# Kernel tuning notes

Measured on AMD Instinct MI355X. Metric: run time of the kernel, lower is better.

## Reference

```python
import jax, jax.numpy as jnp
import numpy as np

TQ, B, H = 1024, 16, 1024   # decoder steps, batch, hidden
S = 4096                     # encoder length


def setup_inputs() -> dict:
    key = jax.random.key(0)
    k1, k2 = jax.random.split(key)
    hiddenState = jax.random.normal(k1, (TQ, B, H), dtype=jnp.float32)
    encoderOut = jax.random.normal(k2, (S, B, H), dtype=jnp.float32)
    return {"hiddenState": hiddenState, "encoderOut": encoderOut}


def reference(hiddenState, encoderOut):
    # encoderOut: [S,B,H] -> [B,S,H]; hiddenState: [Tq,B,H] -> [B,Tq,H]
    # scores[b,s,t] = sum_h enc[b,s,h] * hid[b,t,h]  (bmm of [B,S,H] x [B,H,Tq])
    scores = jnp.einsum('sbh,tbh->bst', encoderOut, hiddenState)  # [B,S,Tq]
    attW = jax.nn.softmax(jnp.tanh(scores), axis=1)  # softmax over encoder axis S
    return attW
```

## Files before the change

kernel.cpp:

```cpp
#include <hip/hip_runtime.h>
#include <hip/hip_bf16.h>

#define TQn 1024
#define Bn  16
#define Hn  1024
#define Sn  4096

#define BM 128
#define BN 128
#define BK 64
#define NKS (Hn / BK)

typedef _Float16 f16x8 __attribute__((ext_vector_type(8)));
typedef float    f32x4 __attribute__((ext_vector_type(4)));

__device__ __forceinline__ void cvt_split(const f32x4& v0, const f32x4& v1,
                                          f16x8& hi, f16x8& lo) {
#pragma unroll
  for (int e = 0; e < 4; ++e) {
    _Float16 h = (_Float16)v0[e];
    hi[e] = h;
    lo[e] = (_Float16)(v0[e] - (float)h);
  }
#pragma unroll
  for (int e = 0; e < 4; ++e) {
    _Float16 h = (_Float16)v1[e];
    hi[4 + e] = h;
    lo[4 + e] = (_Float16)(v1[e] - (float)h);
  }
}

__global__ __launch_bounds__(256, 2)
void att_gemm(const float* __restrict__ hid,
              const float* __restrict__ enc,
              float* __restrict__ out,
              float* __restrict__ sums)
{
  __shared__ f16x8 sAhi[BM * BK / 8];
  __shared__ f16x8 sAlo[BM * BK / 8];
  __shared__ f16x8 sBhi[BN * BK / 8];
  __shared__ f16x8 sBlo[BN * BK / 8];

  const int tid  = threadIdx.x;
  const int lane = tid & 63;
  const int wv   = tid >> 6;
  const int wm   = (wv >> 1) << 6;
  const int wn   = (wv & 1) << 6;

  const int b  = blockIdx.z;
  const int s0 = blockIdx.y * BM;
  const int t0 = blockIdx.x * BN;

  const int unit = tid & 7;
  const int row0 = tid >> 3;

  const float* encB = enc + (size_t)b * Hn;
  const float* hidB = hid + (size_t)b * Hn;
  const size_t ldg = (size_t)Bn * Hn;

  f32x4 acc[4][4];
#pragma unroll
  for (int m = 0; m < 4; ++m)
#pragma unroll
    for (int n = 0; n < 4; ++n)
      acc[m][n] = (f32x4){0.f, 0.f, 0.f, 0.f};

  f32x4 ra[4][2], rb[4][2];

#pragma unroll
  for (int i = 0; i < 4; ++i) {
    const float* pa = encB + (size_t)(s0 + row0 + 32 * i) * ldg + unit * 8;
    ra[i][0] = *(const f32x4*)pa;
    ra[i][1] = *(const f32x4*)(pa + 4);
    const float* pb = hidB + (size_t)(t0 + row0 + 32 * i) * ldg + unit * 8;
    rb[i][0] = *(const f32x4*)pb;
    rb[i][1] = *(const f32x4*)(pb + 4);
  }
#pragma unroll
  for (int i = 0; i < 4; ++i) {
    const int row = row0 + 32 * i;
    const int u   = unit ^ (row & 7);
    f16x8 hi, lo;
    cvt_split(ra[i][0], ra[i][1], hi, lo);
    sAhi[row * 8 + u] = hi;
    sAlo[row * 8 + u] = lo;
    cvt_split(rb[i][0], rb[i][1], hi, lo);
    sBhi[row * 8 + u] = hi;
    sBlo[row * 8 + u] = lo;
  }
  __syncthreads();

#pragma unroll 1
  for (int ks = 0; ks < NKS; ++ks) {
    if (ks + 1 < NKS) {
      const int ko = (ks + 1) * BK;
#pragma unroll
      for (int i = 0; i < 4; ++i) {
        const float* pa = encB + (size_t)(s0 + row0 + 32 * i) * ldg + ko + unit * 8;
        ra[i][0] = *(const f32x4*)pa;
        ra[i][1] = *(const f32x4*)(pa + 4);
        const float* pb = hidB + (size_t)(t0 + row0 + 32 * i) * ldg + ko + unit * 8;
        rb[i][0] = *(const f32x4*)pb;
        rb[i][1] = *(const f32x4*)(pb + 4);
      }
    }

#pragma unroll
    for (int sl = 0; sl < 2; ++sl) {
      const int ko = sl * 4 + (lane >> 4);
      f16x8 ah[4], al[4], bh[4], bl[4];
#pragma unroll
      for (int m = 0; m < 4; ++m) {
        const int r = wm + m * 16 + (lane & 15);
        const int u = ko ^ (r & 7);
        ah[m] = sAhi[r * 8 + u];
        al[m] = sAlo[r * 8 + u];
      }
#pragma unroll
      for (int n = 0; n < 4; ++n) {
        const int r = wn + n * 16 + (lane & 15);
        const int u = ko ^ (r & 7);
        bh[n] = sBhi[r * 8 + u];
        bl[n] = sBlo[r * 8 + u];
      }
#pragma unroll
      for (int m = 0; m < 4; ++m)
#pragma unroll
        for (int n = 0; n < 4; ++n) {
          acc[m][n] = __builtin_amdgcn_mfma_f32_16x16x32_f16(ah[m], bh[n], acc[m][n], 0, 0, 0);
          acc[m][n] = __builtin_amdgcn_mfma_f32_16x16x32_f16(ah[m], bl[n], acc[m][n], 0, 0, 0);
          acc[m][n] = __builtin_amdgcn_mfma_f32_16x16x32_f16(al[m], bh[n], acc[m][n], 0, 0, 0);
        }
    }
    __syncthreads();

    if (ks + 1 < NKS) {
#pragma unroll
      for (int i = 0; i < 4; ++i) {
        const int row = row0 + 32 * i;
        const int u   = unit ^ (row & 7);
        f16x8 hi, lo;
        cvt_split(ra[i][0], ra[i][1], hi, lo);
        sAhi[row * 8 + u] = hi;
        sAlo[row * 8 + u] = lo;
        cvt_split(rb[i][0], rb[i][1], hi, lo);
        sBhi[row * 8 + u] = hi;
        sBlo[row * 8 + u] = lo;
      }
    }
    __syncthreads();
  }

#pragma unroll
  for (int n = 0; n < 4; ++n) {
    const int t = t0 + wn + n * 16 + (lane & 15);
    float csum = 0.f;
#pragma unroll
    for (int m = 0; m < 4; ++m) {
      const int sb = s0 + wm + m * 16 + ((lane >> 4) << 2);
#pragma unroll
      for (int j = 0; j < 4; ++j) {
        const float x  = acc[m][n][j];
        const float w  = __expf(tanhf(x));
        out[((size_t)b * Sn + (sb + j)) * TQn + t] = w;
        csum += w;
      }
    }
    csum += __shfl_xor(csum, 16, 64);
    csum += __shfl_xor(csum, 32, 64);
    if ((lane >> 4) == 0)
      atomicAdd(&sums[b * TQn + t], csum);
  }
}

__global__ void zero_kernel(float* __restrict__ p, int n) {
  int i = blockIdx.x * 256 + threadIdx.x;
  if (i < n) p[i] = 0.f;
}

__global__ void inv_kernel(float* __restrict__ sums, int n) {
  int i = blockIdx.x * 256 + threadIdx.x;
  if (i < n) sums[i] = 1.0f / sums[i];
}

__global__ __launch_bounds__(256)
void scale_kernel(float* __restrict__ out, const float* __restrict__ inv) {
  const int total4 = Bn * Sn * TQn / 4;
  f32x4* o4 = (f32x4*)out;
  const f32x4* i4 = (const f32x4*)inv;
  const int stride = gridDim.x * blockDim.x;
  for (int i = blockIdx.x * blockDim.x + threadIdx.x; i < total4; i += stride) {
    const int tq = i & 255;
    const int bb = i >> 20;
    f32x4 v = o4[i];
    f32x4 s = i4[bb * 256 + tq];
    o4[i] = v * s;
  }
}

extern "C" void kernel_launch(void* const* d_in, const int* in_sizes, int n_in,
                              void* d_out, int out_size, void* d_ws, size_t ws_size,
                              hipStream_t stream) {
  const float* hid = (const float*)d_in[0];
  const float* enc = (const float*)d_in[1];
  float* out  = (float*)d_out;
  float* sums = (float*)d_ws;

  const int nsum = Bn * TQn;
  zero_kernel<<<(nsum + 255) / 256, 256, 0, stream>>>(sums, nsum);

  dim3 grid(TQn / BN, Sn / BM, Bn);
  att_gemm<<<grid, 256, 0, stream>>>(hid, enc, out, sums);

  inv_kernel<<<(nsum + 255) / 256, 256, 0, stream>>>(sums, nsum);

  scale_kernel<<<2048, 256, 0, stream>>>(out, sums);
}
```

Measured before the change: 972.8 us.

## Pre-split inputs into fp16 hi/lo and stream them into LDS directly

Separate conversion kernels now split the fp32 encoder and hidden tensors into fp16 hi/lo arrays in the workspace. A new GEMM kernel then copies tiles straight from global memory into double-buffered LDS with global_load_lds, using BK=32. This removes the conversion work each block repeated on every tile and the register staging between global memory and LDS. In exchange it adds two full conversion passes over the inputs and needs a large workspace; if the workspace is too small, the old kernel runs as a fallback.

```diff
diff --git a/kernel.cpp b/kernel.cpp
--- a/kernel.cpp
+++ b/kernel.cpp
@@ -8,11 +8,19 @@
 
 #define BM 128
 #define BN 128
-#define BK 64
-#define NKS (Hn / BK)
 
 typedef _Float16 f16x8 __attribute__((ext_vector_type(8)));
 typedef float    f32x4 __attribute__((ext_vector_type(4)));
+
+#if defined(__has_builtin)
+#if __has_builtin(__builtin_amdgcn_global_load_lds)
+#define HAVE_GLDS 1
+#else
+#define HAVE_GLDS 0
+#endif
+#else
+#define HAVE_GLDS 0
+#endif
 
 __device__ __forceinline__ void cvt_split(const f32x4& v0, const f32x4& v1,
                                           f16x8& hi, f16x8& lo) {
@@ -30,16 +38,159 @@
   }
 }
 
+
+__global__ __launch_bounds__(256)
+void cvt_kernel(const float* __restrict__ src, _Float16* __restrict__ hi,
+                _Float16* __restrict__ lo, int n8) {
+  const int stride = gridDim.x * blockDim.x;
+  const f32x4* s4 = (const f32x4*)src;
+  f16x8* h8 = (f16x8*)hi;
+  f16x8* l8 = (f16x8*)lo;
+  for (int i = blockIdx.x * blockDim.x + threadIdx.x; i < n8; i += stride) {
+    f32x4 v0 = s4[2 * i];
+    f32x4 v1 = s4[2 * i + 1];
+    f16x8 h, l;
+    cvt_split(v0, v1, h, l);
+    h8[i] = h;
+    l8[i] = l;
+  }
+}
+
+#if HAVE_GLDS
+#define GL(lbase, g) __builtin_amdgcn_global_load_lds( \
+    (const __attribute__((address_space(1))) void*)(g), \
+    (__attribute__((address_space(3))) void*)(lbase), 16, 0, 0)
+#else
+#define GL(lbase, g) (((f16x8*)(lbase))[lane] = *(const f16x8*)(g))
+#endif
+
 __global__ __launch_bounds__(256, 2)
-void att_gemm(const float* __restrict__ hid,
-              const float* __restrict__ enc,
-              float* __restrict__ out,
-              float* __restrict__ sums)
+void att_gemm_f(const _Float16* __restrict__ encHi, const _Float16* __restrict__ encLo,
+                const _Float16* __restrict__ hidHi, const _Float16* __restrict__ hidLo,
+                float* __restrict__ out, float* __restrict__ sums)
 {
-  __shared__ f16x8 sAhi[BM * BK / 8];
-  __shared__ f16x8 sAlo[BM * BK / 8];
-  __shared__ f16x8 sBhi[BN * BK / 8];
-  __shared__ f16x8 sBlo[BN * BK / 8];
+  __shared__ f16x8 sAhi[2][512];
+  __shared__ f16x8 sAlo[2][512];
+  __shared__ f16x8 sBhi[2][512];
+  __shared__ f16x8 sBlo[2][512];
+
+  const int tid  = threadIdx.x;
+  const int lane = tid & 63;
+  const int w    = tid >> 6;
+  const int wm   = (w >> 1) << 6;
+  const int wn   = (w & 1) << 6;
+
+  const int b  = blockIdx.z;
+  const int s0 = blockIdx.y * BM;
+  const int t0 = blockIdx.x * BN;
+
+  const int rl   = lane >> 2;
+  const int uu   = lane & 3;
+  const int row0 = w * 32 + rl;
+  const int row1 = w * 32 + 16 + rl;
+  const int ug0  = uu ^ ((row0 >> 1) & 3);
+  const int ug1  = uu ^ ((row1 >> 1) & 3);
+
+  const size_t offA0 = ((size_t)(s0 + row0) * Bn + b) * Hn + ug0 * 8;
+  const size_t offA1 = ((size_t)(s0 + row1) * Bn + b) * Hn + ug1 * 8;
+  const size_t offB0 = ((size_t)(t0 + row0) * Bn + b) * Hn + ug0 * 8;
+  const size_t offB1 = ((size_t)(t0 + row1) * Bn + b) * Hn + ug1 * 8;
+
+  const int slot0 = w * 128;
+
+  f32x4 acc[4][4];
+#pragma unroll
+  for (int m = 0; m < 4; ++m)
+#pragma unroll
+    for (int n = 0; n < 4; ++n)
+      acc[m][n] = (f32x4){0.f, 0.f, 0.f, 0.f};
+
+#define STAGE(bf, ks) do {                                   \
+    const size_t ko = (size_t)(ks) * 32;                     \
+    GL(&sAhi[bf][slot0],      encHi + offA0 + ko);           \
+    GL(&sAhi[bf][slot0 + 64], encHi + offA1 + ko);           \
+    GL(&sAlo[bf][slot0],      encLo + offA0 + ko);           \
+    GL(&sAlo[bf][slot0 + 64], encLo + offA1 + ko);           \
+    GL(&sBhi[bf][slot0],      hidHi + offB0 + ko);           \
+    GL(&sBhi[bf][slot0 + 64], hidHi + offB1 + ko);           \
+    GL(&sBlo[bf][slot0],      hidLo + offB0 + ko);           \
+    GL(&sBlo[bf][slot0 + 64], hidLo + offB1 + ko);           \
+  } while (0)
+
+#define COMPUTE(bf) do {                                     \
+    const int ko4 = lane >> 4;                               \
+    f16x8 ah[4], al[4], bh[4], bl[4];                        \
+    _Pragma("unroll")                                        \
+    for (int m = 0; m < 4; ++m) {                            \
+      const int r  = wm + m * 16 + (lane & 15);              \
+      const int us = ko4 ^ ((r >> 1) & 3);                   \
+      ah[m] = sAhi[bf][r * 4 + us];                          \
+      al[m] = sAlo[bf][r * 4 + us];                          \
+    }                                                        \
+    _Pragma("unroll")                                        \
+    for (int n = 0; n < 4; ++n) {                            \
+      const int r  = wn + n * 16 + (lane & 15);              \
+      const int us = ko4 ^ ((r >> 1) & 3);                   \
+      bh[n] = sBhi[bf][r * 4 + us];                          \
+      bl[n] = sBlo[bf][r * 4 + us];                          \
+    }                                                        \
+    _Pragma("unroll")                                        \
+    for (int m = 0; m < 4; ++m)                              \
+      _Pragma("unroll")                                      \
+      for (int n = 0; n < 4; ++n) {                          \
+        acc[m][n] = __builtin_amdgcn_mfma_f32_16x16x32_f16(ah[m], bh[n], acc[m][n], 0, 0, 0); \
+        acc[m][n] = __builtin_amdgcn_mfma_f32_16x16x32_f16(ah[m], bl[n], acc[m][n], 0, 0, 0); \
+        acc[m][n] = __builtin_amdgcn_mfma_f32_16x16x32_f16(al[m], bh[n], acc[m][n], 0, 0, 0); \
+      }                                                      \
+  } while (0)
+
+  STAGE(0, 0);
+  __syncthreads();
+
+#pragma unroll 1
+  for (int ks = 0; ks < 32; ++ks) {
+    if (ks < 31) STAGE((ks + 1) & 1, ks + 1);
+    COMPUTE(ks & 1);
+    __syncthreads();
+  }
+
+#undef STAGE
+#undef COMPUTE
+
+#pragma unroll
+  for (int n = 0; n < 4; ++n) {
+    const int t = t0 + wn + n * 16 + (lane & 15);
+    float csum = 0.f;
+#pragma unroll
+    for (int m = 0; m < 4; ++m) {
+      const int sb = s0 + wm + m * 16 + ((lane >> 4) << 2);
+#pragma unroll
+      for (int j = 0; j < 4; ++j) {
+        const float x = acc[m][n][j];
+        const float wgt = __expf(tanhf(x));
+        out[((size_t)b * Sn + (sb + j)) * TQn + t] = wgt;
+        csum += wgt;
+      }
+    }
+    csum += __shfl_xor(csum, 16, 64);
+    csum += __shfl_xor(csum, 32, 64);
+    if ((lane >> 4) == 0)
+      atomicAdd(&sums[b * TQn + t], csum);
+  }
+}
+
+
+#define BKf 64
+#define NKSf (Hn / BKf)
+
+__global__ __launch_bounds__(256, 2)
+void att_gemm_fb(const float* __restrict__ hid, const float* __restrict__ enc,
+                 float* __restrict__ out, float* __restrict__ sums)
+{
+  __shared__ f16x8 sAhi[BM * BKf / 8];
+  __shared__ f16x8 sAlo[BM * BKf / 8];
+  __shared__ f16x8 sBhi[BN * BKf / 8];
+  __shared__ f16x8 sBlo[BN * BKf / 8];
 
   const int tid  = threadIdx.x;
   const int lane = tid & 63;
@@ -91,9 +242,9 @@
   __syncthreads();
 
 #pragma unroll 1
-  for (int ks = 0; ks < NKS; ++ks) {
-    if (ks + 1 < NKS) {
-      const int ko = (ks + 1) * BK;
+  for (int ks = 0; ks < NKSf; ++ks) {
+    if (ks + 1 < NKSf) {
+      const int ko = (ks + 1) * BKf;
 #pragma unroll
       for (int i = 0; i < 4; ++i) {
         const float* pa = encB + (size_t)(s0 + row0 + 32 * i) * ldg + ko + unit * 8;
@@ -104,7 +255,6 @@
         rb[i][1] = *(const f32x4*)(pb + 4);
       }
     }
-
 #pragma unroll
     for (int sl = 0; sl < 2; ++sl) {
       const int ko = sl * 4 + (lane >> 4);
@@ -134,7 +284,7 @@
     }
     __syncthreads();
 
-    if (ks + 1 < NKS) {
+    if (ks + 1 < NKSf) {
 #pragma unroll
       for (int i = 0; i < 4; ++i) {
         const int row = row0 + 32 * i;
@@ -160,10 +310,10 @@
       const int sb = s0 + wm + m * 16 + ((lane >> 4) << 2);
 #pragma unroll
       for (int j = 0; j < 4; ++j) {
-        const float x  = acc[m][n][j];
-        const float w  = __expf(tanhf(x));
-        out[((size_t)b * Sn + (sb + j)) * TQn + t] = w;
-        csum += w;
+        const float x = acc[m][n][j];
+        const float wgt = __expf(tanhf(x));
+        out[((size_t)b * Sn + (sb + j)) * TQn + t] = wgt;
+        csum += wgt;
       }
     }
     csum += __shfl_xor(csum, 16, 64);
@@ -172,6 +322,7 @@
       atomicAdd(&sums[b * TQn + t], csum);
   }
 }
+
 
 __global__ void zero_kernel(float* __restrict__ p, int n) {
   int i = blockIdx.x * 256 + threadIdx.x;
@@ -198,21 +349,39 @@
   }
 }
 
+
 extern "C" void kernel_launch(void* const* d_in, const int* in_sizes, int n_in,
                               void* d_out, int out_size, void* d_ws, size_t ws_size,
                               hipStream_t stream) {
   const float* hid = (const float*)d_in[0];
   const float* enc = (const float*)d_in[1];
-  float* out  = (float*)d_out;
-  float* sums = (float*)d_ws;
+  float* out = (float*)d_out;
+
+  const size_t ENC_N = (size_t)Sn * Bn * Hn;
+  const size_t HID_N = (size_t)TQn * Bn * Hn;
+  const size_t need  = (ENC_N + HID_N) * 4 + 65536;
 
   const int nsum = Bn * TQn;
-  zero_kernel<<<(nsum + 255) / 256, 256, 0, stream>>>(sums, nsum);
-
   dim3 grid(TQn / BN, Sn / BM, Bn);
-  att_gemm<<<grid, 256, 0, stream>>>(hid, enc, out, sums);
-
-  inv_kernel<<<(nsum + 255) / 256, 256, 0, stream>>>(sums, nsum);
-
-  scale_kernel<<<2048, 256, 0, stream>>>(out, sums);
-}
+
+  if (ws_size >= need) {
+    _Float16* encHi = (_Float16*)d_ws;
+    _Float16* encLo = encHi + ENC_N;
+    _Float16* hidHi = encLo + ENC_N;
+    _Float16* hidLo = hidHi + HID_N;
+    float* sums = (float*)(hidLo + HID_N);
+
+    zero_kernel<<<(nsum + 255) / 256, 256, 0, stream>>>(sums, nsum);
+    cvt_kernel<<<2048, 256, 0, stream>>>(enc, encHi, encLo, (int)(ENC_N / 8));
+    cvt_kernel<<<2048, 256, 0, stream>>>(hid, hidHi, hidLo, (int)(HID_N / 8));
+    att_gemm_f<<<grid, 256, 0, stream>>>(encHi, encLo, hidHi, hidLo, out, sums);
+    inv_kernel<<<(nsum + 255) / 256, 256, 0, stream>>>(sums, nsum);
+    scale_kernel<<<2048, 256, 0, stream>>>(out, sums);
+  } else {
+    float* sums = (float*)d_ws;
+    zero_kernel<<<(nsum + 255) / 256, 256, 0, stream>>>(sums, nsum);
+    att_gemm_fb<<<grid, 256, 0, stream>>>(hid, enc, out, sums);
+    inv_kernel<<<(nsum + 255) / 256, 256, 0, stream>>>(sums, nsum);
+    scale_kernel<<<2048, 256, 0, stream>>>(out, sums);
+  }
+}
```

Result: slower. 1.326 ms (+36.3%).
